# Kernel optimization log

Hardware: AMD Instinct MI355X
Metric: run time of the kernel (lower is better)

The kernel has to match this reference:

```python
import jax, jax.numpy as jnp
import numpy as np

N_NODES = 10000
N_EDGES = 160000
HIDDEN = 128


def setup_inputs() -> dict:
    key = jax.random.key(0)
    ks = jax.random.split(key, 7)
    s = 1.0 / np.sqrt(HIDDEN)
    s3 = 1.0 / np.sqrt(3 * HIDDEN)
    return {
        "x": jax.random.normal(ks[0], (N_NODES, 4, HIDDEN), dtype=jnp.float32),
        "edge_index": jax.random.randint(ks[1], (2, N_EDGES), 0, N_NODES, dtype=jnp.int64),
        "W_scalar_rel": jax.random.normal(ks[2], (HIDDEN, HIDDEN), dtype=jnp.float32) * s,
        "W_scalar_root": jax.random.normal(ks[3], (HIDDEN, HIDDEN), dtype=jnp.float32) * s,
        "b_scalar_root": jax.random.normal(ks[4], (HIDDEN,), dtype=jnp.float32) * s,
        "W_vector_rel": jax.random.normal(ks[5], (3 * HIDDEN, 3 * HIDDEN), dtype=jnp.float32) * s3,
        "W_vector_root": jax.random.normal(ks[6], (3 * HIDDEN, 3 * HIDDEN), dtype=jnp.float32) * s3,
    }


def reference(x, edge_index, W_scalar_rel, W_scalar_root, b_scalar_root,
              W_vector_rel, W_vector_root):
    n = x.shape[0]
    scalar = x[:, 0, :]                       # [N, H]
    vector = x[:, 1:, :].reshape(n, -1)       # [N, 3H]
    row, col = edge_index[0], edge_index[1]
    # gather source node features, linear transform (torch Linear: y = x @ W.T)
    scalar_msg = scalar[col] @ W_scalar_rel.T  # [E, H]
    vector_msg = vector[col] @ W_vector_rel.T  # [E, 3H]
    # scatter-add aggregation to destination nodes
    scalar_agg = jax.ops.segment_sum(scalar_msg, row, num_segments=n)
    vector_agg = jax.ops.segment_sum(vector_msg, row, num_segments=n)
    scalar_out = scalar @ W_scalar_root.T + b_scalar_root + scalar_agg  # [N, H]
    vector_out = (vector @ W_vector_root.T + vector_agg).reshape(n, 3, -1)
    return jnp.concatenate([scalar_out[:, None, :], vector_out], axis=1)  # [N, 4, H]
```

## Files before the change

### kernel.cpp

```cpp
#include <hip/hip_runtime.h>
#include <stdint.h>

typedef unsigned short u16;
typedef unsigned int u32;
typedef __attribute__((ext_vector_type(4))) float floatx4;
typedef __attribute__((ext_vector_type(8))) short short8;


static __device__ __forceinline__ float bfhi2f(u32 hi) {
    union { u32 i; float f; } v; v.i = hi; return v.f;
}
static __device__ __forceinline__ u16 f2bf(float f) {
    union { float f; u32 i; } v; v.f = f;
    u32 r = v.i + 0x7fffu + ((v.i >> 16) & 1u);
    return (u16)(r >> 16);
}
static __device__ __forceinline__ uint4 pack8(const float* s) {
    float4 a = *(const float4*)s, b = *(const float4*)(s + 4);
    uint4 p;
    p.x = (u32)f2bf(a.x) | ((u32)f2bf(a.y) << 16);
    p.y = (u32)f2bf(a.z) | ((u32)f2bf(a.w) << 16);
    p.z = (u32)f2bf(b.x) | ((u32)f2bf(b.y) << 16);
    p.w = (u32)f2bf(b.z) | ((u32)f2bf(b.w) << 16);
    return p;
}


__global__ __launch_bounds__(256) void prep_kernel(
        const float* __restrict__ x, u16* __restrict__ xb, int n8,
        const float* __restrict__ w2, const float* __restrict__ w3,
        const float* __restrict__ w5, const float* __restrict__ w6,
        u16* __restrict__ Wb, int s2, int s5, int nw8,
        const int* __restrict__ ei, int E, int N, int* __restrict__ counts,
        int nb_x, int nb_w) {
    const int b = blockIdx.x, tid = threadIdx.x;
    if (b < nb_x) {
        int t = b * 256 + tid;
        if (t < n8) *(uint4*)(xb + (size_t)t * 8) = pack8(x + (size_t)t * 8);
    } else if (b < nb_x + nb_w) {
        int t = (b - nb_x) * 256 + tid;
        if (t < nw8) {
            int g = t * 8;
            const float* src; int loc;
            if (g < s2)               { src = w2; loc = g; }
            else if (g < 2 * s2)      { src = w3; loc = g - s2; }
            else if (g < 2 * s2 + s5) { src = w5; loc = g - 2 * s2; }
            else                      { src = w6; loc = g - 2 * s2 - s5; }
            *(uint4*)(Wb + g) = pack8(src + loc);
        }
    } else {
        int e = (b - nb_x - nb_w) * 256 + tid;
        if (e < E) {
            unsigned r = (unsigned)ei[e];
            unsigned c = (unsigned)ei[E + e];
            if (r < (unsigned)N && c < (unsigned)N) atomicAdd(&counts[r], 1);
        }
    }
}


__global__ void scan_kernel(const int* __restrict__ counts, int* __restrict__ offsets,
                            int* __restrict__ cursor, int n) {
    __shared__ int part[16];
    __shared__ int carry;
    const int tid = threadIdx.x, lane = tid & 63, wave = tid >> 6;
    if (tid == 0) carry = 0;
    __syncthreads();
    for (int base = 0; base < n; base += 1024) {
        int i = base + tid;
        int v = (i < n) ? counts[i] : 0;
        int s = v;
#pragma unroll
        for (int d = 1; d < 64; d <<= 1) {
            int t = __shfl_up(s, d);
            if (lane >= d) s += t;
        }
        if (lane == 63) part[wave] = s;
        __syncthreads();
        if (tid < 16) {
            int p = part[tid];
#pragma unroll
            for (int d = 1; d < 16; d <<= 1) {
                int t = __shfl_up(p, d);
                if (tid >= d) p += t;
            }
            part[tid] = p;
        }
        __syncthreads();
        int c0 = carry;
        int woff = wave ? part[wave - 1] : 0;
        int excl = c0 + woff + s - v;
        if (i < n) { offsets[i] = excl; cursor[i] = excl; }
        int tot = part[15];
        __syncthreads();
        if (tid == 0) carry = c0 + tot;
    }
    __syncthreads();
    if (tid == 0) offsets[n] = carry;
}

__global__ void fill_kernel(const int* __restrict__ ei, int E, int N,
                            int* __restrict__ cursor, int* __restrict__ edge_dst) {
    int e = blockIdx.x * blockDim.x + threadIdx.x;
    if (e >= E) return;
    unsigned r = (unsigned)ei[e];
    unsigned c = (unsigned)ei[E + e];
    if (r < (unsigned)N && c < (unsigned)N) {
        int p = atomicAdd(&cursor[r], 1);
        edge_dst[p] = (int)c;
    }
}


static __device__ __forceinline__ void acc8(float* acc, uint4 d) {
    acc[0] += bfhi2f(d.x << 16); acc[1] += bfhi2f(d.x & 0xffff0000u);
    acc[2] += bfhi2f(d.y << 16); acc[3] += bfhi2f(d.y & 0xffff0000u);
    acc[4] += bfhi2f(d.z << 16); acc[5] += bfhi2f(d.z & 0xffff0000u);
    acc[6] += bfhi2f(d.w << 16); acc[7] += bfhi2f(d.w & 0xffff0000u);
}

__global__ __launch_bounds__(256) void gather_kernel(
        const u16* __restrict__ xb, const int* __restrict__ offsets,
        const int* __restrict__ edge_dst, u16* __restrict__ agg, int N) {
    int gw   = (blockIdx.x * 256 + threadIdx.x) >> 6;
    int lane = threadIdx.x & 63;
    if (gw >= N) return;
    const int beg = offsets[gw], end = offsets[gw + 1];
    float acc[8] = {0.f,0.f,0.f,0.f,0.f,0.f,0.f,0.f};
    const u16* xl = xb + (size_t)lane * 8;
    int e = beg;
    for (; e + 8 <= end; e += 8) {
        int c[8];
#pragma unroll
        for (int u = 0; u < 8; ++u) c[u] = edge_dst[e + u];
        uint4 d[8];
#pragma unroll
        for (int u = 0; u < 8; ++u) d[u] = *(const uint4*)(xl + (size_t)c[u] * 512);
#pragma unroll
        for (int u = 0; u < 8; ++u) acc8(acc, d[u]);
    }
    for (; e < end; ++e) {
        int c = edge_dst[e];
        acc8(acc, *(const uint4*)(xl + (size_t)c * 512));
    }
    uint4 p;
    p.x = (u32)f2bf(acc[0]) | ((u32)f2bf(acc[1]) << 16);
    p.y = (u32)f2bf(acc[2]) | ((u32)f2bf(acc[3]) << 16);
    p.z = (u32)f2bf(acc[4]) | ((u32)f2bf(acc[5]) << 16);
    p.w = (u32)f2bf(acc[6]) | ((u32)f2bf(acc[7]) << 16);
    *(uint4*)(agg + (size_t)gw * 512 + (size_t)lane * 8) = p;
}


#define LP 72

__global__ __launch_bounds__(256, 4) void gemm_kernel(
        const u16* __restrict__ xb, const u16* __restrict__ agg,
        const u16* __restrict__ Wb, const float* __restrict__ bias,
        int s2, int s5, float* __restrict__ out, int N) {
    const int unit = blockIdx.y;
    const bool is_scalar = (unit < 2);

    const int Kw      = is_scalar ? 128 : 384;
    const int K       = 2 * Kw;
    const int selfOff = is_scalar ? 0 : 128;
    const int j0      = is_scalar ? unit * 64 : (unit - 2) * 64;
    const int outOff  = is_scalar ? 0 : 128;
    const u16* Wrel   = is_scalar ? Wb : (Wb + 2 * s2);
    const u16* Wroot  = is_scalar ? (Wb + s2) : (Wb + 2 * s2 + s5);

    __shared__ u16 As[64 * LP];
    __shared__ u16 Bs[64 * LP];

    const int row0 = blockIdx.x * 64;
    const int tid  = threadIdx.x;
    const int lane = tid & 63, wid = tid >> 6;
    const int mBase = (wid >> 1) * 32, nBase = (wid & 1) * 32;
    const int lrow = lane & 15;
    const int lchunk = (lane >> 4) * 8;

    floatx4 acc[2][2];
#pragma unroll
    for (int i = 0; i < 2; ++i)
#pragma unroll
        for (int j = 0; j < 2; ++j) acc[i][j] = (floatx4){0.f, 0.f, 0.f, 0.f};

    for (int k0 = 0; k0 < K; k0 += 64) {
        const bool selfPhase = (k0 < Kw);
        const int ks   = selfPhase ? k0 : (k0 - Kw);
        const int acol = selfOff + ks;
        const u16* Asrc = selfPhase ? xb : agg;
        const u16* Wsrc = selfPhase ? Wroot : Wrel;
#pragma unroll
        for (int it = 0; it < 2; ++it) {
            int ci = it * 256 + tid;
            int r = ci >> 3, cc = (ci & 7) << 3;
            int ar = row0 + r; if (ar >= N) ar = N - 1;
            *(uint4*)&As[r * LP + cc] =
                *(const uint4*)(Asrc + (size_t)ar * 512 + acol + cc);
            *(uint4*)&Bs[r * LP + cc] =
                *(const uint4*)(Wsrc + (size_t)(j0 + r) * Kw + ks + cc);
        }
        __syncthreads();
#pragma unroll
        for (int kk = 0; kk < 64; kk += 32) {
            short8 a[2], b[2];
#pragma unroll
            for (int i = 0; i < 2; ++i)
                a[i] = *(const short8*)&As[(mBase + i * 16 + lrow) * LP + kk + lchunk];
#pragma unroll
            for (int j = 0; j < 2; ++j)
                b[j] = *(const short8*)&Bs[(nBase + j * 16 + lrow) * LP + kk + lchunk];
#pragma unroll
            for (int i = 0; i < 2; ++i)
#pragma unroll
                for (int j = 0; j < 2; ++j)
                    acc[i][j] = __builtin_amdgcn_mfma_f32_16x16x32_bf16(a[i], b[j], acc[i][j], 0, 0, 0);
        }
        __syncthreads();
    }

    const int lcol = lane & 15;
    const int lrow4 = (lane >> 4) * 4;
#pragma unroll
    for (int i = 0; i < 2; ++i) {
#pragma unroll
        for (int j = 0; j < 2; ++j) {
            int col = nBase + j * 16 + lcol;
            float bv = is_scalar ? bias[j0 + col] : 0.f;
#pragma unroll
            for (int r = 0; r < 4; ++r) {
                int row = row0 + mBase + i * 16 + lrow4 + r;
                if (row < N)
                    out[(size_t)row * 512 + outOff + j0 + col] = acc[i][j][r] + bv;
            }
        }
    }
}

extern "C" void kernel_launch(void* const* d_in, const int* in_sizes, int n_in,
                              void* d_out, int out_size, void* d_ws, size_t ws_size,
                              hipStream_t stream) {
    const float* x      = (const float*)d_in[0];
    const int*   ei     = (const int*)d_in[1];
    const float* Wsrel  = (const float*)d_in[2];
    const float* Wsroot = (const float*)d_in[3];
    const float* bs     = (const float*)d_in[4];
    const float* Wvrel  = (const float*)d_in[5];
    const float* Wvroot = (const float*)d_in[6];
    float* out = (float*)d_out;

    const int N  = in_sizes[0] / 512;
    const int E  = in_sizes[1] / 2;
    const int s2 = in_sizes[2];
    const int s5 = in_sizes[5];
    const int Nx = in_sizes[0];
    const int Mt = (N + 63) / 64;

    char* ws = (char*)d_ws;
    size_t off = 0;
    int* counts = (int*)(ws + off);   off += (size_t)N * 4;        off = (off + 255) & ~(size_t)255;
    int* offsets = (int*)(ws + off);  off += (size_t)(N + 1) * 4;  off = (off + 255) & ~(size_t)255;
    int* cursor = (int*)(ws + off);   off += (size_t)N * 4;        off = (off + 255) & ~(size_t)255;
    int* edge_dst = (int*)(ws + off); off += (size_t)E * 4;        off = (off + 255) & ~(size_t)255;
    u16* Wb = (u16*)(ws + off);       off += (size_t)(2*s2 + 2*s5) * 2; off = (off + 255) & ~(size_t)255;
    u16* agg = (u16*)(ws + off);      off += (size_t)Nx * 2;       off = (off + 255) & ~(size_t)255;
    u16* x_bf = (u16*)(ws + off);

    const int n8   = Nx / 8;
    const int nw8  = (2 * s2 + 2 * s5) / 8;
    const int nb_x = (n8 + 255) / 256;
    const int nb_w = (nw8 + 255) / 256;
    const int nb_c = (E + 255) / 256;

    hipMemsetAsync(counts, 0, (size_t)N * 4, stream);
    prep_kernel<<<nb_x + nb_w + nb_c, 256, 0, stream>>>(
        x, x_bf, n8, Wsrel, Wsroot, Wvrel, Wvroot, Wb, s2, s5, nw8,
        ei, E, N, counts, nb_x, nb_w);
    scan_kernel<<<1, 1024, 0, stream>>>(counts, offsets, cursor, N);
    fill_kernel<<<(E + 255) / 256, 256, 0, stream>>>(ei, E, N, cursor, edge_dst);
    gather_kernel<<<(N * 64 + 255) / 256, 256, 0, stream>>>(x_bf, offsets, edge_dst, agg, N);
    dim3 grid(Mt, 8);
    gemm_kernel<<<grid, 256, 0, stream>>>(x_bf, agg, Wb, bs, s2, s5, out, N);
}
```

Before: 161.3 us.

## Widen GEMM K-tile, unroll gather with shuffled indices, and vectorize scan

The GEMM now stages a 128-wide K slice per iteration instead of 64, with the LDS row pitch enlarged to match, which halves the number of sync barriers and loop iterations. The gather kernel loads 16 edge indices per wave with a single load and broadcasts them via shuffles, keeping 16 row loads in flight, and adds 8- and 4-edge tail steps. The scan kernel has each thread handle four counts per pass. In exchange the GEMM uses twice the LDS, which may lower occupancy, and the gather holds more registers.

```diff
diff --git a/kernel.cpp b/kernel.cpp
--- a/kernel.cpp
+++ b/kernel.cpp
@@ -66,31 +66,38 @@
     const int tid = threadIdx.x, lane = tid & 63, wave = tid >> 6;
     if (tid == 0) carry = 0;
     __syncthreads();
-    for (int base = 0; base < n; base += 1024) {
-        int i = base + tid;
-        int v = (i < n) ? counts[i] : 0;
-        int s = v;
+    for (int base = 0; base < n; base += 4096) {
+        int i0 = base + tid * 4;
+        int a0 = (i0     < n) ? counts[i0]     : 0;
+        int a1 = (i0 + 1 < n) ? counts[i0 + 1] : 0;
+        int a2 = (i0 + 2 < n) ? counts[i0 + 2] : 0;
+        int a3 = (i0 + 3 < n) ? counts[i0 + 3] : 0;
+        int s0 = a0, s1 = s0 + a1, s2 = s1 + a2, s3 = s2 + a3;
+        int t = s3;
 #pragma unroll
         for (int d = 1; d < 64; d <<= 1) {
-            int t = __shfl_up(s, d);
-            if (lane >= d) s += t;
-        }
-        if (lane == 63) part[wave] = s;
+            int q = __shfl_up(t, d);
+            if (lane >= d) t += q;
+        }
+        if (lane == 63) part[wave] = t;
         __syncthreads();
         if (tid < 16) {
             int p = part[tid];
 #pragma unroll
             for (int d = 1; d < 16; d <<= 1) {
-                int t = __shfl_up(p, d);
-                if (tid >= d) p += t;
+                int q = __shfl_up(p, d);
+                if (tid >= d) p += q;
             }
             part[tid] = p;
         }
         __syncthreads();
         int c0 = carry;
         int woff = wave ? part[wave - 1] : 0;
-        int excl = c0 + woff + s - v;
-        if (i < n) { offsets[i] = excl; cursor[i] = excl; }
+        int tbase = c0 + woff + (t - s3);
+        if (i0     < n) { offsets[i0]     = tbase;      cursor[i0]     = tbase; }
+        if (i0 + 1 < n) { offsets[i0 + 1] = tbase + s0; cursor[i0 + 1] = tbase + s0; }
+        if (i0 + 2 < n) { offsets[i0 + 2] = tbase + s1; cursor[i0 + 2] = tbase + s1; }
+        if (i0 + 3 < n) { offsets[i0 + 3] = tbase + s2; cursor[i0 + 3] = tbase + s2; }
         int tot = part[15];
         __syncthreads();
         if (tid == 0) carry = c0 + tot;
@@ -129,15 +136,40 @@
     float acc[8] = {0.f,0.f,0.f,0.f,0.f,0.f,0.f,0.f};
     const u16* xl = xb + (size_t)lane * 8;
     int e = beg;
-    for (; e + 8 <= end; e += 8) {
-        int c[8];
-#pragma unroll
-        for (int u = 0; u < 8; ++u) c[u] = edge_dst[e + u];
+    for (; e + 16 <= end; e += 16) {
+        int myid = edge_dst[e + (lane & 15)];
+        uint4 d[16];
+#pragma unroll
+        for (int u = 0; u < 16; ++u) {
+            int c = __shfl(myid, u);
+            d[u] = *(const uint4*)(xl + (size_t)c * 512);
+        }
+#pragma unroll
+        for (int u = 0; u < 16; ++u) acc8(acc, d[u]);
+    }
+    if (e + 8 <= end) {
+        int myid = edge_dst[e + (lane & 7)];
         uint4 d[8];
 #pragma unroll
-        for (int u = 0; u < 8; ++u) d[u] = *(const uint4*)(xl + (size_t)c[u] * 512);
+        for (int u = 0; u < 8; ++u) {
+            int c = __shfl(myid, u);
+            d[u] = *(const uint4*)(xl + (size_t)c * 512);
+        }
 #pragma unroll
         for (int u = 0; u < 8; ++u) acc8(acc, d[u]);
+        e += 8;
+    }
+    if (e + 4 <= end) {
+        int myid = edge_dst[e + (lane & 3)];
+        uint4 d[4];
+#pragma unroll
+        for (int u = 0; u < 4; ++u) {
+            int c = __shfl(myid, u);
+            d[u] = *(const uint4*)(xl + (size_t)c * 512);
+        }
+#pragma unroll
+        for (int u = 0; u < 4; ++u) acc8(acc, d[u]);
+        e += 4;
     }
     for (; e < end; ++e) {
         int c = edge_dst[e];
@@ -152,7 +184,7 @@
 }
 
 
-#define LP 72
+#define LP 136
 
 __global__ __launch_bounds__(256, 4) void gemm_kernel(
         const u16* __restrict__ xb, const u16* __restrict__ agg,
@@ -185,16 +217,16 @@
 #pragma unroll
         for (int j = 0; j < 2; ++j) acc[i][j] = (floatx4){0.f, 0.f, 0.f, 0.f};
 
-    for (int k0 = 0; k0 < K; k0 += 64) {
+    for (int k0 = 0; k0 < K; k0 += 128) {
         const bool selfPhase = (k0 < Kw);
         const int ks   = selfPhase ? k0 : (k0 - Kw);
         const int acol = selfOff + ks;
         const u16* Asrc = selfPhase ? xb : agg;
         const u16* Wsrc = selfPhase ? Wroot : Wrel;
 #pragma unroll
-        for (int it = 0; it < 2; ++it) {
+        for (int it = 0; it < 4; ++it) {
             int ci = it * 256 + tid;
-            int r = ci >> 3, cc = (ci & 7) << 3;
+            int r = ci >> 4, cc = (ci & 15) << 3;
             int ar = row0 + r; if (ar >= N) ar = N - 1;
             *(uint4*)&As[r * LP + cc] =
                 *(const uint4*)(Asrc + (size_t)ar * 512 + acol + cc);
@@ -203,7 +235,7 @@
         }
         __syncthreads();
 #pragma unroll
-        for (int kk = 0; kk < 64; kk += 32) {
+        for (int kk = 0; kk < 128; kk += 32) {
             short8 a[2], b[2];
 #pragma unroll
             for (int i = 0; i < 2; ++i)
```

Result: faster. 157.7 us (-2.3%).
